# Kernel tuning notes

Measured on AMD Instinct MI355X. Metric: run time of the kernel, lower is better.

Reference implementation:

```python
import jax, jax.numpy as jnp
import numpy as np

S, N, F, DEG, D_IN, D_OUT = 8, 50000, 5, 32, 128, 128


def setup_inputs() -> dict:
    key = jax.random.key(0)
    k1, k2, k3, k4, k5 = jax.random.split(key, 5)
    std = 1.0 / np.sqrt(D_OUT)
    x = jax.random.normal(k1, (S, N, F), dtype=jnp.float32)
    neigh_idx = jax.random.randint(k2, (S, N, DEG), 0, N, dtype=jnp.int32)
    W_1 = jax.random.uniform(k3, (F, D_IN), minval=-std, maxval=std, dtype=jnp.float32)
    W = jax.random.uniform(k4, (2 * D_IN, D_OUT), minval=-std, maxval=std, dtype=jnp.float32)
    b = jax.random.uniform(k5, (D_OUT,), minval=-std, maxval=std, dtype=jnp.float32)
    return {"x": x, "neigh_idx": neigh_idx, "W_1": W_1, "W": W, "b": b}


def reference(x, neigh_idx, W_1, W, b):
    # Self features projected through W_1 (the x_ list in the torch code).
    self_feats = jnp.einsum('snf,fd->snd', x, W_1)          # [S, N, D_IN]
    # Aggregator: mean over sampled neighbors' raw features (per sample).
    gathered = jax.vmap(lambda xs, ids: xs[ids])(x, neigh_idx)  # [S, N, DEG, F]
    neigh_raw = gathered.mean(axis=2)                        # [S, N, F]
    neigh_feats = jnp.einsum('snf,fd->snd', neigh_raw, W_1)  # [S, N, D_IN]
    # combine == 'concat'
    combined = jnp.concatenate([self_feats, neigh_feats], axis=-1)  # [S, N, 2*D_IN]
    y = jnp.einsum('snc,co->sno', combined, W) + b           # [S, N, D_OUT]
    return jax.nn.relu(y)
```

## Files before the change

### kernel.cpp

```cpp
#include <hip/hip_runtime.h>
#include <cstddef>
#include <cstdint>

static constexpr int S_    = 8;
static constexpr int N_    = 50000;
static constexpr int F_    = 5;
static constexpr int DEG_  = 32;
static constexpr int DOUT_ = 128;
static constexpr int TOTAL_NODES = S_ * N_;
static constexpr int NODES_PER_WAVE = 16;
static constexpr int GROUPS = TOTAL_NODES / NODES_PER_WAVE;

typedef float    f32x4 __attribute__((ext_vector_type(4)));
typedef int      i32x2 __attribute__((ext_vector_type(2)));
typedef int      i32x4 __attribute__((ext_vector_type(4)));
typedef _Float16 h2    __attribute__((ext_vector_type(2)));

__global__ void wc_precompute(const float* __restrict__ W1,
                              const float* __restrict__ W,
                              float* __restrict__ Wc) {
    int t = blockIdx.x * blockDim.x + threadIdx.x;
    if (t >= 2 * F_ * DOUT_) return;
    int o = t & (DOUT_ - 1);
    int f = (t >> 7) % F_;
    int p = t / (F_ * DOUT_);
    const float* w1r  = W1 + f * 128;
    const float* wcol = W + (size_t)p * 128 * DOUT_ + o;
    float acc = 0.f;
#pragma unroll 8
    for (int d = 0; d < 128; ++d)
        acc = fmaf(w1r[d], wcol[(size_t)d * DOUT_], acc);
    Wc[t] = acc;
}

__global__ __launch_bounds__(256) void xpack_fp8(const float* __restrict__ x,
                                                 i32x2* __restrict__ xq) {
    int t = blockIdx.x * blockDim.x + threadIdx.x;
    if (t >= TOTAL_NODES) return;
    const float* r = x + (size_t)t * F_;
    int d0 = __builtin_amdgcn_cvt_pk_fp8_f32(r[0], r[1], 0, false);
    d0     = __builtin_amdgcn_cvt_pk_fp8_f32(r[2], r[3], d0, true);
    int d1 = __builtin_amdgcn_cvt_pk_fp8_f32(r[4], 0.f, 0, false);
    i32x2 v; v.x = d0; v.y = d1;
    xq[t] = v;
}

struct alignas(16) H8 { _Float16 v[8]; };

__global__ __launch_bounds__(256) void xpack_f16(const float* __restrict__ x,
                                                 H8* __restrict__ xh) {
    int t = blockIdx.x * blockDim.x + threadIdx.x;
    if (t >= TOTAL_NODES) return;
    const float* r = x + (size_t)t * F_;
    H8 o;
#pragma unroll
    for (int f = 0; f < F_; ++f) o.v[f] = (_Float16)r[f];
#pragma unroll
    for (int f = F_; f < 8; ++f) o.v[f] = (_Float16)0.f;
    xh[t] = o;
}

__global__ __launch_bounds__(256) void encoder_v6(
    const int*   __restrict__ idx,
    const i32x2* __restrict__ xq,
    const H8*    __restrict__ xh,
    const float* __restrict__ Wc,
    const float* __restrict__ b,
    float* __restrict__ out) {
    const int lane = threadIdx.x & 63;
    const int sl   = lane & 31;
    const int half = lane >> 5;
    const int o0   = sl << 2;
    const int g    = (blockIdx.x * blockDim.x + threadIdx.x) >> 6;

    float wa[F_][4], wb[F_][4];
#pragma unroll
    for (int f = 0; f < F_; ++f) {
        f32x4 a  = *reinterpret_cast<const f32x4*>(Wc + f * DOUT_ + o0);
        f32x4 bb = *reinterpret_cast<const f32x4*>(Wc + F_ * DOUT_ + f * DOUT_ + o0);
        wa[f][0] = a.x;  wa[f][1] = a.y;  wa[f][2] = a.z;  wa[f][3] = a.w;
        wb[f][0] = bb.x; wb[f][1] = bb.y; wb[f][2] = bb.z; wb[f][3] = bb.w;
    }
    const f32x4 bias = *reinterpret_cast<const f32x4*>(b + o0);
    const float inv = 1.f / DEG_;

    const int base = g * NODES_PER_WAVE;
    const int s    = base / N_;
    const i32x2* xs = xq + (size_t)s * N_;

    int nb[8];
#pragma unroll
    for (int j = 0; j < 8; ++j) {
        const int node = base + 2 * j + half;
        nb[j] = __builtin_nontemporal_load(idx + (size_t)node * DEG_ + sl);
    }
    i32x2 gq[8];
#pragma unroll
    for (int j = 0; j < 8; ++j) gq[j] = xs[nb[j]];
    union US { i32x4 i; h2 h[4]; } sv[8];
#pragma unroll
    for (int j = 0; j < 8; ++j) {
        const int node = base + 2 * j + half;
        sv[j].i = *reinterpret_cast<const i32x4*>(xh + node);
    }

#pragma unroll
    for (int j = 0; j < 8; ++j) {
        const int d0 = gq[j].x, d1 = gq[j].y;
        const float g0 = __builtin_amdgcn_cvt_f32_fp8(d0, 0);
        const float g1 = __builtin_amdgcn_cvt_f32_fp8(d0, 1);
        const float g2 = __builtin_amdgcn_cvt_f32_fp8(d0, 2);
        const float g3 = __builtin_amdgcn_cvt_f32_fp8(d0, 3);
        const float g4 = __builtin_amdgcn_cvt_f32_fp8(d1, 0);
        h2 v0 = { (_Float16)g0, (_Float16)g1 };
        h2 v1 = { (_Float16)g2, (_Float16)g3 };
        h2 v2 = { (_Float16)g4, (_Float16)0.f };
#pragma unroll
        for (int m = 1; m < 32; m <<= 1) {
            v0 += __builtin_bit_cast(h2, __shfl_xor(__builtin_bit_cast(int, v0), m));
            v1 += __builtin_bit_cast(h2, __shfl_xor(__builtin_bit_cast(int, v1), m));
            v2 += __builtin_bit_cast(h2, __shfl_xor(__builtin_bit_cast(int, v2), m));
        }
        const float nf[F_] = { (float)v0.x * inv, (float)v0.y * inv,
                               (float)v1.x * inv, (float)v1.y * inv,
                               (float)v2.x * inv };
        const float sf[F_] = { (float)sv[j].h[0].x, (float)sv[j].h[0].y,
                               (float)sv[j].h[1].x, (float)sv[j].h[1].y,
                               (float)sv[j].h[2].x };
        float y0 = bias.x, y1 = bias.y, y2 = bias.z, y3 = bias.w;
#pragma unroll
        for (int f = 0; f < F_; ++f) {
            y0 = fmaf(sf[f], wa[f][0], y0); y0 = fmaf(nf[f], wb[f][0], y0);
            y1 = fmaf(sf[f], wa[f][1], y1); y1 = fmaf(nf[f], wb[f][1], y1);
            y2 = fmaf(sf[f], wa[f][2], y2); y2 = fmaf(nf[f], wb[f][2], y2);
            y3 = fmaf(sf[f], wa[f][3], y3); y3 = fmaf(nf[f], wb[f][3], y3);
        }
        const int node = base + 2 * j + half;
        f32x4 yv = { fmaxf(y0, 0.f), fmaxf(y1, 0.f), fmaxf(y2, 0.f), fmaxf(y3, 0.f) };
        __builtin_nontemporal_store(yv,
            reinterpret_cast<f32x4*>(out + (size_t)node * DOUT_ + o0));
    }
}

__global__ __launch_bounds__(256) void encoder_f32(
    const float* __restrict__ x, const int* __restrict__ idx,
    const float* __restrict__ Wc, const float* __restrict__ b,
    float* __restrict__ out, int total_pairs) {
    const int lane = threadIdx.x & 63;
    const int sl   = lane & 31;
    const int half = lane >> 5;
    const int o0   = sl << 2;
    const int gwave  = (blockIdx.x * blockDim.x + threadIdx.x) >> 6;
    const int nwaves = (gridDim.x * blockDim.x) >> 6;
    float wa[F_][4], wb[F_][4];
#pragma unroll
    for (int f = 0; f < F_; ++f) {
        f32x4 a  = *reinterpret_cast<const f32x4*>(Wc + f * DOUT_ + o0);
        f32x4 bb = *reinterpret_cast<const f32x4*>(Wc + F_ * DOUT_ + f * DOUT_ + o0);
        wa[f][0] = a.x;  wa[f][1] = a.y;  wa[f][2] = a.z;  wa[f][3] = a.w;
        wb[f][0] = bb.x; wb[f][1] = bb.y; wb[f][2] = bb.z; wb[f][3] = bb.w;
    }
    const f32x4 bias = *reinterpret_cast<const f32x4*>(b + o0);
    for (int p = gwave; p < total_pairs; p += nwaves) {
        const int node = p * 2 + half;
        const int s    = node / N_;
        const int nb = idx[(size_t)node * DEG_ + sl];
        const float* xr = x + ((size_t)s * N_ + nb) * F_;
        float n0 = xr[0], n1 = xr[1], n2 = xr[2], n3 = xr[3], n4 = xr[4];
#pragma unroll
        for (int m = 1; m < 32; m <<= 1) {
            n0 += __shfl_xor(n0, m); n1 += __shfl_xor(n1, m); n2 += __shfl_xor(n2, m);
            n3 += __shfl_xor(n3, m); n4 += __shfl_xor(n4, m);
        }
        const float inv = 1.f / DEG_;
        const float nf[F_] = {n0 * inv, n1 * inv, n2 * inv, n3 * inv, n4 * inv};
        const float* xsp = x + (size_t)node * F_;
        const float sf[F_] = {xsp[0], xsp[1], xsp[2], xsp[3], xsp[4]};
        float y0 = bias.x, y1 = bias.y, y2 = bias.z, y3 = bias.w;
#pragma unroll
        for (int f = 0; f < F_; ++f) {
            y0 = fmaf(sf[f], wa[f][0], y0); y0 = fmaf(nf[f], wb[f][0], y0);
            y1 = fmaf(sf[f], wa[f][1], y1); y1 = fmaf(nf[f], wb[f][1], y1);
            y2 = fmaf(sf[f], wa[f][2], y2); y2 = fmaf(nf[f], wb[f][2], y2);
            y3 = fmaf(sf[f], wa[f][3], y3); y3 = fmaf(nf[f], wb[f][3], y3);
        }
        f32x4 yv = { fmaxf(y0, 0.f), fmaxf(y1, 0.f), fmaxf(y2, 0.f), fmaxf(y3, 0.f) };
        *reinterpret_cast<f32x4*>(out + (size_t)node * DOUT_ + o0) = yv;
    }
}

extern "C" void kernel_launch(void* const* d_in, const int* in_sizes, int n_in,
                              void* d_out, int out_size, void* d_ws, size_t ws_size,
                              hipStream_t stream) {
    const float* x   = (const float*)d_in[0];
    const int*   idx = (const int*)  d_in[1];
    const float* W1  = (const float*)d_in[2];
    const float* W   = (const float*)d_in[3];
    const float* b   = (const float*)d_in[4];
    float* out = (float*)d_out;

    const size_t wc_bytes = (size_t)2 * F_ * DOUT_ * sizeof(float);
    const size_t xq_bytes = (size_t)TOTAL_NODES * sizeof(i32x2);
    const size_t xh_bytes = (size_t)TOTAL_NODES * sizeof(H8);
    float* Wc = (float*)d_ws;

    hipLaunchKernelGGL(wc_precompute, dim3(5), dim3(256), 0, stream, W1, W, Wc);

    if (ws_size >= wc_bytes + xq_bytes + xh_bytes) {
        i32x2* xq = (i32x2*)((char*)d_ws + wc_bytes);
        H8*    xh = (H8*)   ((char*)d_ws + wc_bytes + xq_bytes);
        hipLaunchKernelGGL(xpack_fp8, dim3((TOTAL_NODES + 255) / 256), dim3(256),
                           0, stream, x, xq);
        hipLaunchKernelGGL(xpack_f16, dim3((TOTAL_NODES + 255) / 256), dim3(256),
                           0, stream, x, xh);
        hipLaunchKernelGGL(encoder_v6, dim3(GROUPS / 4), dim3(256), 0, stream,
                           idx, xq, xh, Wc, b, out);
    } else {
        hipLaunchKernelGGL(encoder_f32, dim3(2048), dim3(256), 0, stream,
                           x, idx, Wc, b, out, TOTAL_NODES / 2);
    }
}
```

Baseline: 115.4 us.

## Restructure encoder to per-lane neighbor sums via LDS and drop f16 pack kernel

Each lane now owns one node. It loads that node's 32 neighbor indices as vector loads, gathers the fp8 features, and sums them in fp32 registers. This replaces the cross-lane fp16 shuffle reduction. Per-node sums go through shared memory, and a second phase writes 128-wide outputs with self features read straight from fp32 x, so the xpack_f16 kernel launch is removed. The 1/DEG scale is folded into the weights. The cost is more work per wave (64 nodes), a block barrier, and strided per-lane index loads that are less coalesced.

```diff
diff --git a/kernel.cpp b/kernel.cpp
--- a/kernel.cpp
+++ b/kernel.cpp
@@ -8,13 +8,12 @@
 static constexpr int DEG_  = 32;
 static constexpr int DOUT_ = 128;
 static constexpr int TOTAL_NODES = S_ * N_;
-static constexpr int NODES_PER_WAVE = 16;
-static constexpr int GROUPS = TOTAL_NODES / NODES_PER_WAVE;
-
-typedef float    f32x4 __attribute__((ext_vector_type(4)));
-typedef int      i32x2 __attribute__((ext_vector_type(2)));
-typedef int      i32x4 __attribute__((ext_vector_type(4)));
-typedef _Float16 h2    __attribute__((ext_vector_type(2)));
+static constexpr int NPW = 64;
+static constexpr int NWAVES_T = TOTAL_NODES / NPW;
+
+typedef float f32x4 __attribute__((ext_vector_type(4)));
+typedef int   i32x2 __attribute__((ext_vector_type(2)));
+typedef int   i32x4 __attribute__((ext_vector_type(4)));
 
 __global__ void wc_precompute(const float* __restrict__ W1,
                               const float* __restrict__ W,
@@ -45,98 +44,90 @@
     xq[t] = v;
 }
 
-struct alignas(16) H8 { _Float16 v[8]; };
-
-__global__ __launch_bounds__(256) void xpack_f16(const float* __restrict__ x,
-                                                 H8* __restrict__ xh) {
-    int t = blockIdx.x * blockDim.x + threadIdx.x;
-    if (t >= TOTAL_NODES) return;
-    const float* r = x + (size_t)t * F_;
-    H8 o;
-#pragma unroll
-    for (int f = 0; f < F_; ++f) o.v[f] = (_Float16)r[f];
-#pragma unroll
-    for (int f = F_; f < 8; ++f) o.v[f] = (_Float16)0.f;
-    xh[t] = o;
-}
-
-__global__ __launch_bounds__(256) void encoder_v6(
+__global__ __launch_bounds__(128) void encoder_v8(
     const int*   __restrict__ idx,
     const i32x2* __restrict__ xq,
-    const H8*    __restrict__ xh,
+    const float* __restrict__ x,
     const float* __restrict__ Wc,
     const float* __restrict__ b,
     float* __restrict__ out) {
+    __shared__ float lds_sum[2][NPW * F_];
+    const int wv   = threadIdx.x >> 6;
     const int lane = threadIdx.x & 63;
+    const int g    = blockIdx.x * 2 + wv;
+    const int base = g * NPW;
+
+    {
+        const int node = base + lane;
+        const int s    = node / N_;
+        const i32x2* __restrict__ xs  = xq + (size_t)s * N_;
+        const int*   __restrict__ irow = idx + (size_t)node * DEG_;
+
+        i32x4 nbv[8];
+#pragma unroll
+        for (int t = 0; t < 8; ++t)
+            nbv[t] = __builtin_nontemporal_load(
+                         reinterpret_cast<const i32x4*>(irow) + t);
+
+        float a0 = 0.f, a1 = 0.f, a2 = 0.f, a3 = 0.f, a4 = 0.f;
+#pragma unroll
+        for (int c = 0; c < 4; ++c) {
+            i32x2 q[8];
+#pragma unroll
+            for (int u = 0; u < 8; ++u) {
+                const int k = c * 8 + u;
+                q[u] = xs[nbv[k >> 2][k & 3]];
+            }
+#pragma unroll
+            for (int u = 0; u < 8; ++u) {
+                const int d0 = q[u].x, d1 = q[u].y;
+                a0 += __builtin_amdgcn_cvt_f32_fp8(d0, 0);
+                a1 += __builtin_amdgcn_cvt_f32_fp8(d0, 1);
+                a2 += __builtin_amdgcn_cvt_f32_fp8(d0, 2);
+                a3 += __builtin_amdgcn_cvt_f32_fp8(d0, 3);
+                a4 += __builtin_amdgcn_cvt_f32_fp8(d1, 0);
+            }
+        }
+        float* ls = &lds_sum[wv][lane * F_];
+        ls[0] = a0; ls[1] = a1; ls[2] = a2; ls[3] = a3; ls[4] = a4;
+    }
+    __syncthreads();
+
     const int sl   = lane & 31;
     const int half = lane >> 5;
     const int o0   = sl << 2;
-    const int g    = (blockIdx.x * blockDim.x + threadIdx.x) >> 6;
+    const float inv = 1.f / DEG_;
 
     float wa[F_][4], wb[F_][4];
 #pragma unroll
     for (int f = 0; f < F_; ++f) {
         f32x4 a  = *reinterpret_cast<const f32x4*>(Wc + f * DOUT_ + o0);
         f32x4 bb = *reinterpret_cast<const f32x4*>(Wc + F_ * DOUT_ + f * DOUT_ + o0);
-        wa[f][0] = a.x;  wa[f][1] = a.y;  wa[f][2] = a.z;  wa[f][3] = a.w;
-        wb[f][0] = bb.x; wb[f][1] = bb.y; wb[f][2] = bb.z; wb[f][3] = bb.w;
+        wa[f][0] = a.x;        wa[f][1] = a.y;
+        wa[f][2] = a.z;        wa[f][3] = a.w;
+        wb[f][0] = bb.x * inv; wb[f][1] = bb.y * inv;
+        wb[f][2] = bb.z * inv; wb[f][3] = bb.w * inv;
     }
     const f32x4 bias = *reinterpret_cast<const f32x4*>(b + o0);
-    const float inv = 1.f / DEG_;
-
-    const int base = g * NODES_PER_WAVE;
-    const int s    = base / N_;
-    const i32x2* xs = xq + (size_t)s * N_;
-
-    int nb[8];
-#pragma unroll
-    for (int j = 0; j < 8; ++j) {
-        const int node = base + 2 * j + half;
-        nb[j] = __builtin_nontemporal_load(idx + (size_t)node * DEG_ + sl);
-    }
-    i32x2 gq[8];
-#pragma unroll
-    for (int j = 0; j < 8; ++j) gq[j] = xs[nb[j]];
-    union US { i32x4 i; h2 h[4]; } sv[8];
-#pragma unroll
-    for (int j = 0; j < 8; ++j) {
-        const int node = base + 2 * j + half;
-        sv[j].i = *reinterpret_cast<const i32x4*>(xh + node);
-    }
-
-#pragma unroll
-    for (int j = 0; j < 8; ++j) {
-        const int d0 = gq[j].x, d1 = gq[j].y;
-        const float g0 = __builtin_amdgcn_cvt_f32_fp8(d0, 0);
-        const float g1 = __builtin_amdgcn_cvt_f32_fp8(d0, 1);
-        const float g2 = __builtin_amdgcn_cvt_f32_fp8(d0, 2);
-        const float g3 = __builtin_amdgcn_cvt_f32_fp8(d0, 3);
-        const float g4 = __builtin_amdgcn_cvt_f32_fp8(d1, 0);
-        h2 v0 = { (_Float16)g0, (_Float16)g1 };
-        h2 v1 = { (_Float16)g2, (_Float16)g3 };
-        h2 v2 = { (_Float16)g4, (_Float16)0.f };
-#pragma unroll
-        for (int m = 1; m < 32; m <<= 1) {
-            v0 += __builtin_bit_cast(h2, __shfl_xor(__builtin_bit_cast(int, v0), m));
-            v1 += __builtin_bit_cast(h2, __shfl_xor(__builtin_bit_cast(int, v1), m));
-            v2 += __builtin_bit_cast(h2, __shfl_xor(__builtin_bit_cast(int, v2), m));
-        }
-        const float nf[F_] = { (float)v0.x * inv, (float)v0.y * inv,
-                               (float)v1.x * inv, (float)v1.y * inv,
-                               (float)v2.x * inv };
-        const float sf[F_] = { (float)sv[j].h[0].x, (float)sv[j].h[0].y,
-                               (float)sv[j].h[1].x, (float)sv[j].h[1].y,
-                               (float)sv[j].h[2].x };
+
+#pragma unroll 4
+    for (int i = 0; i < NPW / 2; ++i) {
+        const int nloc = 2 * i + half;
+        const int node = base + nloc;
+        const float* __restrict__ xr = x + (size_t)node * F_;
+        const float* __restrict__ ms = &lds_sum[wv][nloc * F_];
         float y0 = bias.x, y1 = bias.y, y2 = bias.z, y3 = bias.w;
 #pragma unroll
         for (int f = 0; f < F_; ++f) {
-            y0 = fmaf(sf[f], wa[f][0], y0); y0 = fmaf(nf[f], wb[f][0], y0);
-            y1 = fmaf(sf[f], wa[f][1], y1); y1 = fmaf(nf[f], wb[f][1], y1);
-            y2 = fmaf(sf[f], wa[f][2], y2); y2 = fmaf(nf[f], wb[f][2], y2);
-            y3 = fmaf(sf[f], wa[f][3], y3); y3 = fmaf(nf[f], wb[f][3], y3);
-        }
-        const int node = base + 2 * j + half;
-        f32x4 yv = { fmaxf(y0, 0.f), fmaxf(y1, 0.f), fmaxf(y2, 0.f), fmaxf(y3, 0.f) };
+            const float sf = xr[f];
+            const float nf = ms[f];
+            y0 = fmaf(sf, wa[f][0], y0); y0 = fmaf(nf, wb[f][0], y0);
+            y1 = fmaf(sf, wa[f][1], y1); y1 = fmaf(nf, wb[f][1], y1);
+            y2 = fmaf(sf, wa[f][2], y2); y2 = fmaf(nf, wb[f][2], y2);
+            y3 = fmaf(sf, wa[f][3], y3); y3 = fmaf(nf, wb[f][3], y3);
+        }
+        f32x4 yv = { fmaxf(y0, 0.f), fmaxf(y1, 0.f),
+                     fmaxf(y2, 0.f), fmaxf(y3, 0.f) };
         __builtin_nontemporal_store(yv,
             reinterpret_cast<f32x4*>(out + (size_t)node * DOUT_ + o0));
     }
@@ -201,20 +192,16 @@
 
     const size_t wc_bytes = (size_t)2 * F_ * DOUT_ * sizeof(float);
     const size_t xq_bytes = (size_t)TOTAL_NODES * sizeof(i32x2);
-    const size_t xh_bytes = (size_t)TOTAL_NODES * sizeof(H8);
     float* Wc = (float*)d_ws;
 
     hipLaunchKernelGGL(wc_precompute, dim3(5), dim3(256), 0, stream, W1, W, Wc);
 
-    if (ws_size >= wc_bytes + xq_bytes + xh_bytes) {
+    if (ws_size >= wc_bytes + xq_bytes) {
         i32x2* xq = (i32x2*)((char*)d_ws + wc_bytes);
-        H8*    xh = (H8*)   ((char*)d_ws + wc_bytes + xq_bytes);
         hipLaunchKernelGGL(xpack_fp8, dim3((TOTAL_NODES + 255) / 256), dim3(256),
                            0, stream, x, xq);
-        hipLaunchKernelGGL(xpack_f16, dim3((TOTAL_NODES + 255) / 256), dim3(256),
-                           0, stream, x, xh);
-        hipLaunchKernelGGL(encoder_v6, dim3(GROUPS / 4), dim3(256), 0, stream,
-                           idx, xq, xh, Wc, b, out);
+        hipLaunchKernelGGL(encoder_v8, dim3(NWAVES_T / 2), dim3(128), 0, stream,
+                           idx, xq, x, Wc, b, out);
     } else {
         hipLaunchKernelGGL(encoder_f32, dim3(2048), dim3(256), 0, stream,
                            x, idx, Wc, b, out, TOTAL_NODES / 2);
```

After: 134.2 us. +16.3%, slower.

## Fuse x packing kernels, use DPP reductions, and double nodes per wave

Applied to the files above, without the earlier changes.

Merges the fp8 and fp16 packing kernels into one pass that reads x once and writes both packed copies. The encoder now handles 32 nodes per wave instead of 16, issuing all index and gather loads up front. It replaces four of the five shuffle-xor reduction steps with DPP row-rotate adds and folds the 1/DEG scale into the neighbor weights. The sample index is recomputed per chunk because a wave's nodes can now span a sample boundary. Together these aim to cut a kernel launch, redundant reads of x, and shuffle overhead, at the cost of more registers per thread and fewer waves in flight.

```diff
diff --git a/kernel.cpp b/kernel.cpp
--- a/kernel.cpp
+++ b/kernel.cpp
@@ -8,13 +8,19 @@
 static constexpr int DEG_  = 32;
 static constexpr int DOUT_ = 128;
 static constexpr int TOTAL_NODES = S_ * N_;
-static constexpr int NODES_PER_WAVE = 16;
-static constexpr int GROUPS = TOTAL_NODES / NODES_PER_WAVE;
+static constexpr int NPW = 32;
+static constexpr int NCH = NPW / 2;
+static constexpr int TOTAL_WAVES = TOTAL_NODES / NPW;
 
 typedef float    f32x4 __attribute__((ext_vector_type(4)));
 typedef int      i32x2 __attribute__((ext_vector_type(2)));
 typedef int      i32x4 __attribute__((ext_vector_type(4)));
 typedef _Float16 h2    __attribute__((ext_vector_type(2)));
+
+#define ROR_ADD(v, CTRL)                                                      \
+    { int t_ = __builtin_amdgcn_update_dpp(                                   \
+          0, __builtin_bit_cast(int, v), (CTRL), 0xF, 0xF, true);             \
+      v += __builtin_bit_cast(h2, t_); }
 
 __global__ void wc_precompute(const float* __restrict__ W1,
                               const float* __restrict__ W,
@@ -33,34 +39,28 @@
     Wc[t] = acc;
 }
 
-__global__ __launch_bounds__(256) void xpack_fp8(const float* __restrict__ x,
-                                                 i32x2* __restrict__ xq) {
+struct alignas(16) H8 { _Float16 v[8]; };
+
+__global__ __launch_bounds__(256) void xpack_both(const float* __restrict__ x,
+                                                  i32x2* __restrict__ xq,
+                                                  H8* __restrict__ xh) {
     int t = blockIdx.x * blockDim.x + threadIdx.x;
     if (t >= TOTAL_NODES) return;
     const float* r = x + (size_t)t * F_;
-    int d0 = __builtin_amdgcn_cvt_pk_fp8_f32(r[0], r[1], 0, false);
-    d0     = __builtin_amdgcn_cvt_pk_fp8_f32(r[2], r[3], d0, true);
-    int d1 = __builtin_amdgcn_cvt_pk_fp8_f32(r[4], 0.f, 0, false);
-    i32x2 v; v.x = d0; v.y = d1;
-    xq[t] = v;
-}
-
-struct alignas(16) H8 { _Float16 v[8]; };
-
-__global__ __launch_bounds__(256) void xpack_f16(const float* __restrict__ x,
-                                                 H8* __restrict__ xh) {
-    int t = blockIdx.x * blockDim.x + threadIdx.x;
-    if (t >= TOTAL_NODES) return;
-    const float* r = x + (size_t)t * F_;
+    const float r0 = r[0], r1 = r[1], r2 = r[2], r3 = r[3], r4 = r[4];
+    int d0 = __builtin_amdgcn_cvt_pk_fp8_f32(r0, r1, 0, false);
+    d0     = __builtin_amdgcn_cvt_pk_fp8_f32(r2, r3, d0, true);
+    int d1 = __builtin_amdgcn_cvt_pk_fp8_f32(r4, 0.f, 0, false);
+    i32x2 q; q.x = d0; q.y = d1;
+    xq[t] = q;
     H8 o;
-#pragma unroll
-    for (int f = 0; f < F_; ++f) o.v[f] = (_Float16)r[f];
-#pragma unroll
-    for (int f = F_; f < 8; ++f) o.v[f] = (_Float16)0.f;
+    o.v[0] = (_Float16)r0; o.v[1] = (_Float16)r1; o.v[2] = (_Float16)r2;
+    o.v[3] = (_Float16)r3; o.v[4] = (_Float16)r4;
+    o.v[5] = (_Float16)0.f; o.v[6] = (_Float16)0.f; o.v[7] = (_Float16)0.f;
     xh[t] = o;
 }
 
-__global__ __launch_bounds__(256) void encoder_v6(
+__global__ __launch_bounds__(256) void encoder_v9(
     const int*   __restrict__ idx,
     const i32x2* __restrict__ xq,
     const H8*    __restrict__ xh,
@@ -71,74 +71,80 @@
     const int sl   = lane & 31;
     const int half = lane >> 5;
     const int o0   = sl << 2;
-    const int g    = (blockIdx.x * blockDim.x + threadIdx.x) >> 6;
-
+    const int w    = (blockIdx.x * blockDim.x + threadIdx.x) >> 6;
+    const int base = w * NPW;
+
+    const float inv = 1.f / DEG_;
     float wa[F_][4], wb[F_][4];
 #pragma unroll
     for (int f = 0; f < F_; ++f) {
         f32x4 a  = *reinterpret_cast<const f32x4*>(Wc + f * DOUT_ + o0);
         f32x4 bb = *reinterpret_cast<const f32x4*>(Wc + F_ * DOUT_ + f * DOUT_ + o0);
-        wa[f][0] = a.x;  wa[f][1] = a.y;  wa[f][2] = a.z;  wa[f][3] = a.w;
-        wb[f][0] = bb.x; wb[f][1] = bb.y; wb[f][2] = bb.z; wb[f][3] = bb.w;
+        wa[f][0] = a.x;        wa[f][1] = a.y;
+        wa[f][2] = a.z;        wa[f][3] = a.w;
+        wb[f][0] = bb.x * inv; wb[f][1] = bb.y * inv;
+        wb[f][2] = bb.z * inv; wb[f][3] = bb.w * inv;
     }
     const f32x4 bias = *reinterpret_cast<const f32x4*>(b + o0);
-    const float inv = 1.f / DEG_;
-
-    const int base = g * NODES_PER_WAVE;
-    const int s    = base / N_;
-    const i32x2* xs = xq + (size_t)s * N_;
-
-    int nb[8];
-#pragma unroll
-    for (int j = 0; j < 8; ++j) {
+
+    int nb[NCH];
+#pragma unroll
+    for (int j = 0; j < NCH; ++j) {
         const int node = base + 2 * j + half;
         nb[j] = __builtin_nontemporal_load(idx + (size_t)node * DEG_ + sl);
     }
-    i32x2 gq[8];
-#pragma unroll
-    for (int j = 0; j < 8; ++j) gq[j] = xs[nb[j]];
-    union US { i32x4 i; h2 h[4]; } sv[8];
-#pragma unroll
-    for (int j = 0; j < 8; ++j) {
-        const int node = base + 2 * j + half;
-        sv[j].i = *reinterpret_cast<const i32x4*>(xh + node);
-    }
-
-#pragma unroll
-    for (int j = 0; j < 8; ++j) {
-        const int d0 = gq[j].x, d1 = gq[j].y;
-        const float g0 = __builtin_amdgcn_cvt_f32_fp8(d0, 0);
-        const float g1 = __builtin_amdgcn_cvt_f32_fp8(d0, 1);
-        const float g2 = __builtin_amdgcn_cvt_f32_fp8(d0, 2);
-        const float g3 = __builtin_amdgcn_cvt_f32_fp8(d0, 3);
-        const float g4 = __builtin_amdgcn_cvt_f32_fp8(d1, 0);
-        h2 v0 = { (_Float16)g0, (_Float16)g1 };
-        h2 v1 = { (_Float16)g2, (_Float16)g3 };
-        h2 v2 = { (_Float16)g4, (_Float16)0.f };
-#pragma unroll
-        for (int m = 1; m < 32; m <<= 1) {
-            v0 += __builtin_bit_cast(h2, __shfl_xor(__builtin_bit_cast(int, v0), m));
-            v1 += __builtin_bit_cast(h2, __shfl_xor(__builtin_bit_cast(int, v1), m));
-            v2 += __builtin_bit_cast(h2, __shfl_xor(__builtin_bit_cast(int, v2), m));
-        }
-        const float nf[F_] = { (float)v0.x * inv, (float)v0.y * inv,
-                               (float)v1.x * inv, (float)v1.y * inv,
-                               (float)v2.x * inv };
-        const float sf[F_] = { (float)sv[j].h[0].x, (float)sv[j].h[0].y,
-                               (float)sv[j].h[1].x, (float)sv[j].h[1].y,
-                               (float)sv[j].h[2].x };
-        float y0 = bias.x, y1 = bias.y, y2 = bias.z, y3 = bias.w;
-#pragma unroll
-        for (int f = 0; f < F_; ++f) {
-            y0 = fmaf(sf[f], wa[f][0], y0); y0 = fmaf(nf[f], wb[f][0], y0);
-            y1 = fmaf(sf[f], wa[f][1], y1); y1 = fmaf(nf[f], wb[f][1], y1);
-            y2 = fmaf(sf[f], wa[f][2], y2); y2 = fmaf(nf[f], wb[f][2], y2);
-            y3 = fmaf(sf[f], wa[f][3], y3); y3 = fmaf(nf[f], wb[f][3], y3);
-        }
-        const int node = base + 2 * j + half;
-        f32x4 yv = { fmaxf(y0, 0.f), fmaxf(y1, 0.f), fmaxf(y2, 0.f), fmaxf(y3, 0.f) };
-        __builtin_nontemporal_store(yv,
-            reinterpret_cast<f32x4*>(out + (size_t)node * DOUT_ + o0));
+    i32x2 gq[NCH];
+#pragma unroll
+    for (int j = 0; j < NCH; ++j) {
+        const int s = (base + 2 * j) / N_;
+        gq[j] = xq[(size_t)s * N_ + nb[j]];
+    }
+
+#pragma unroll
+    for (int bt = 0; bt < 4; ++bt) {
+        union US { i32x4 i; h2 h[4]; } sv[4];
+#pragma unroll
+        for (int u = 0; u < 4; ++u) {
+            const int node = base + 2 * (4 * bt + u) + half;
+            sv[u].i = *reinterpret_cast<const i32x4*>(xh + node);
+        }
+#pragma unroll
+        for (int u = 0; u < 4; ++u) {
+            const int j  = 4 * bt + u;
+            const int d0 = gq[j].x, d1 = gq[j].y;
+            h2 v0 = { (_Float16)__builtin_amdgcn_cvt_f32_fp8(d0, 0),
+                      (_Float16)__builtin_amdgcn_cvt_f32_fp8(d0, 1) };
+            h2 v1 = { (_Float16)__builtin_amdgcn_cvt_f32_fp8(d0, 2),
+                      (_Float16)__builtin_amdgcn_cvt_f32_fp8(d0, 3) };
+            h2 v2 = { (_Float16)__builtin_amdgcn_cvt_f32_fp8(d1, 0),
+                      (_Float16)0.f };
+            ROR_ADD(v0, 0x121); ROR_ADD(v1, 0x121); ROR_ADD(v2, 0x121);
+            ROR_ADD(v0, 0x122); ROR_ADD(v1, 0x122); ROR_ADD(v2, 0x122);
+            ROR_ADD(v0, 0x124); ROR_ADD(v1, 0x124); ROR_ADD(v2, 0x124);
+            ROR_ADD(v0, 0x128); ROR_ADD(v1, 0x128); ROR_ADD(v2, 0x128);
+            v0 += __builtin_bit_cast(h2, __shfl_xor(__builtin_bit_cast(int, v0), 16));
+            v1 += __builtin_bit_cast(h2, __shfl_xor(__builtin_bit_cast(int, v1), 16));
+            v2 += __builtin_bit_cast(h2, __shfl_xor(__builtin_bit_cast(int, v2), 16));
+
+            const float nf[F_] = { (float)v0.x, (float)v0.y,
+                                   (float)v1.x, (float)v1.y, (float)v2.x };
+            const float sf[F_] = { (float)sv[u].h[0].x, (float)sv[u].h[0].y,
+                                   (float)sv[u].h[1].x, (float)sv[u].h[1].y,
+                                   (float)sv[u].h[2].x };
+            float y0 = bias.x, y1 = bias.y, y2 = bias.z, y3 = bias.w;
+#pragma unroll
+            for (int f = 0; f < F_; ++f) {
+                y0 = fmaf(sf[f], wa[f][0], y0); y0 = fmaf(nf[f], wb[f][0], y0);
+                y1 = fmaf(sf[f], wa[f][1], y1); y1 = fmaf(nf[f], wb[f][1], y1);
+                y2 = fmaf(sf[f], wa[f][2], y2); y2 = fmaf(nf[f], wb[f][2], y2);
+                y3 = fmaf(sf[f], wa[f][3], y3); y3 = fmaf(nf[f], wb[f][3], y3);
+            }
+            const int node = base + 2 * j + half;
+            f32x4 yv = { fmaxf(y0, 0.f), fmaxf(y1, 0.f),
+                         fmaxf(y2, 0.f), fmaxf(y3, 0.f) };
+            __builtin_nontemporal_store(yv,
+                reinterpret_cast<f32x4*>(out + (size_t)node * DOUT_ + o0));
+        }
     }
 }
 
@@ -209,11 +215,9 @@
     if (ws_size >= wc_bytes + xq_bytes + xh_bytes) {
         i32x2* xq = (i32x2*)((char*)d_ws + wc_bytes);
         H8*    xh = (H8*)   ((char*)d_ws + wc_bytes + xq_bytes);
-        hipLaunchKernelGGL(xpack_fp8, dim3((TOTAL_NODES + 255) / 256), dim3(256),
-                           0, stream, x, xq);
-        hipLaunchKernelGGL(xpack_f16, dim3((TOTAL_NODES + 255) / 256), dim3(256),
-                           0, stream, x, xh);
-        hipLaunchKernelGGL(encoder_v6, dim3(GROUPS / 4), dim3(256), 0, stream,
+        hipLaunchKernelGGL(xpack_both, dim3((TOTAL_NODES + 255) / 256), dim3(256),
+                           0, stream, x, xq, xh);
+        hipLaunchKernelGGL(encoder_v9, dim3(TOTAL_WAVES / 4), dim3(256), 0, stream,
                            idx, xq, xh, Wc, b, out);
     } else {
         hipLaunchKernelGGL(encoder_f32, dim3(2048), dim3(256), 0, stream,
```

After: 119.5 us. 1.04x slower.
